# Optimization experiments

Measured on AMD Instinct MI355X. Metric: run time of the kernel, lower is better.

Reference implementation:

```python
import jax, jax.numpy as jnp
import numpy as np

EPS = 1e-5  # BatchNorm3d default eps


def setup_inputs() -> dict:
    key = jax.random.key(0)
    ks = jax.random.split(key, 8)
    B, C, T, H, W = 2, 256, 8, 28, 28
    P, NS = 128, 5
    sc = 0.02  # keep activations stable through 5 residual stages
    return {
        "x": jax.random.normal(ks[0], (B, C, T, H, W), jnp.float32),
        "Wt": jax.random.normal(ks[1], (P, C), jnp.float32) * sc,
        "Wp": jax.random.normal(ks[2], (P, C), jnp.float32) * sc,
        "Wg": jax.random.normal(ks[3], (NS, P, C), jnp.float32) * sc,
        "W1": jax.random.normal(ks[4], (NS, C, P), jnp.float32) * sc,
        "W2": jax.random.normal(ks[5], (NS, C, P), jnp.float32) * sc,
        "gamma": jnp.ones((NS, C), jnp.float32),
        "beta": jnp.zeros((NS, C), jnp.float32),
    }


def _batchnorm(x, g, b):
    # x: [B, C, S]; training-mode BN over (batch, spatial) per channel
    mu = jnp.mean(x, axis=(0, 2), keepdims=True)
    var = jnp.var(x, axis=(0, 2), keepdims=True)
    xn = (x - mu) * jax.lax.rsqrt(var + EPS)
    return xn * g[None, :, None] + b[None, :, None]


def reference(x, Wt, Wp, Wg, W1, W2, gamma, beta):
    B, C, T, H, W = x.shape
    S = T * H * W
    xf = x.reshape(B, C, S)                      # [B,C,S]
    # DotKernel: att[b,i,j] = softmax_j( t[b,i,:] . p[b,:,j] )
    t = jnp.einsum("bcs,pc->bsp", xf, Wt)        # [B,S,P]
    p = jnp.einsum("bcs,pc->bps", xf, Wp)        # [B,P,S]
    att = jax.nn.softmax(jnp.einsum("bsp,bpq->bsq", t, p), axis=-1)  # [B,S,S]

    out = xf
    n_stages = Wg.shape[0]
    for i in range(n_stages):  # small fixed stage count
        g = jnp.einsum("bcs,pc->bsp", out, Wg[i])          # [B,S,P]
        x1 = jnp.einsum("bsp,cp->bcs", g, W1[i])           # w_1(g)
        x2 = jnp.einsum("bsq,bqp->bsp", att, g)            # att @ g
        x2 = jnp.einsum("bsp,cp->bcs", x2, W2[i])          # w_2(...)
        out = _batchnorm(x1 + x2, gamma[i], beta[i]) + out  # BN + residual
    return out.reshape(B, C, T, H, W)
```

## Files before the change

### kernel.cpp

```cpp
#include <hip/hip_runtime.h>

#define B_  2
#define C_  256
#define S_  6272
#define P_  128
#define NS_ 5
#define KS_ 7
#define KCH_ 896
#define EPS_ 1e-5f

typedef __attribute__((ext_vector_type(8))) short short8;
typedef __attribute__((ext_vector_type(4))) float f32x4;

__device__ __forceinline__ ushort f2bf(float f) {
    union { float f; unsigned u; } v; v.f = f;
    unsigned r = v.u + 0x7fffu + ((v.u >> 16) & 1u);
    return (ushort)(r >> 16);
}
__device__ __forceinline__ float bf2f(ushort h) {
    union { unsigned u; float f; } v; v.u = ((unsigned)h) << 16;
    return v.f;
}

__global__ void k_convert_weights(const float* __restrict__ Wt, const float* __restrict__ Wp,
                                  const float* __restrict__ Wg, const float* __restrict__ W1,
                                  const float* __restrict__ W2,
                                  ushort* __restrict__ Wtb, ushort* __restrict__ Wpb,
                                  ushort* __restrict__ Wgb, ushort* __restrict__ catb) {
    int i = blockIdx.x * 256 + threadIdx.x;
    const int nWt  = P_ * C_;
    const int nWg  = NS_ * P_ * C_;
    const int nCat = NS_ * C_ * 2 * P_;
    if (i < nWt) { Wtb[i] = f2bf(Wt[i]); Wpb[i] = f2bf(Wp[i]); }
    if (i < nWg) { Wgb[i] = f2bf(Wg[i]); }
    if (i < nCat) {
        int k  = i & 255;
        int c  = (i >> 8) & (C_ - 1);
        int st = i >> 16;
        float v = (k < P_) ? W1[((size_t)st * C_ + c) * P_ + k]
                           : W2[((size_t)st * C_ + c) * P_ + (k - P_)];
        catb[i] = f2bf(v);
    }
}

__global__ void k_init_x(const float* __restrict__ x, float* __restrict__ out,
                         ushort* __restrict__ xb_sc) {
    int bc = blockIdx.x;
    int b = bc / C_, c = bc - b * C_;
    const float* xr = x + (long)bc * S_;
    float* orow = out + (long)bc * S_;
    ushort* xs = xb_sc + (long)b * S_ * C_;
    for (int s = threadIdx.x; s < S_; s += 256) {
        float v = xr[s];
        orow[s] = v;
        xs[(long)s * C_ + c] = f2bf(v);
    }
}

template <int MODE>
__global__ __launch_bounds__(256, 2)
void k_gemm(const ushort* __restrict__ A, const ushort* __restrict__ Bm,
            void* __restrict__ Out, ushort* __restrict__ OutT,
            int M, int N, int K, int lda, int ldb, int ldo, int ldot,
            long sA, long sB, long sO, long sOT, int nks, int kch) {
    const int z = blockIdx.z;
    const int b = z / nks, ch = z - b * nks;
    A  += (long)b * sA;
    Bm += (long)b * sB;
    const int k0 = ch * kch, k1 = k0 + kch;

    const int bm = blockIdx.x * 128, bn = blockIdx.y * 128;

    __shared__ ushort Al[128][40];
    __shared__ ushort Bl[128][40];

    const int tid = threadIdx.x, lane = tid & 63, wid = tid >> 6;
    const int wr = (wid >> 1) * 64, wc = (wid & 1) * 64;
    const int r16 = lane & 15, kg = lane >> 4;

    f32x4 acc[4][4];
    #pragma unroll
    for (int i = 0; i < 4; ++i)
        #pragma unroll
        for (int j = 0; j < 4; ++j)
            acc[i][j] = (f32x4){0.f, 0.f, 0.f, 0.f};

    for (int kk = k0; kk < k1; kk += 32) {
        {
            int u = tid;         int r = u >> 2, c8 = (u & 3) << 3;
            *(short8*)&Al[r][c8] = *(const short8*)&A[(long)(bm + r) * lda + kk + c8];
        }
        {
            int u = tid + 256;   int r = u >> 2, c8 = (u & 3) << 3;
            *(short8*)&Al[r][c8] = *(const short8*)&A[(long)(bm + r) * lda + kk + c8];
        }
        {
            int u = tid;         int r = u >> 2, c8 = (u & 3) << 3;
            *(short8*)&Bl[r][c8] = *(const short8*)&Bm[(long)(bn + r) * ldb + kk + c8];
        }
        {
            int u = tid + 256;   int r = u >> 2, c8 = (u & 3) << 3;
            *(short8*)&Bl[r][c8] = *(const short8*)&Bm[(long)(bn + r) * ldb + kk + c8];
        }
        __syncthreads();

        short8 af[4], bfv[4];
        #pragma unroll
        for (int i = 0; i < 4; ++i)
            af[i] = *(const short8*)&Al[wr + i * 16 + r16][kg * 8];
        #pragma unroll
        for (int j = 0; j < 4; ++j)
            bfv[j] = *(const short8*)&Bl[wc + j * 16 + r16][kg * 8];

        #pragma unroll
        for (int i = 0; i < 4; ++i)
            #pragma unroll
            for (int j = 0; j < 4; ++j)
                acc[i][j] = __builtin_amdgcn_mfma_f32_16x16x32_bf16(af[i], bfv[j], acc[i][j], 0, 0, 0);
        __syncthreads();
    }

    const int orow0 = bm + wr + kg * 4;
    const int ocol0 = bn + wc + r16;
    if (MODE == 2) {
        float* O = (float*)Out + (long)z * sO;
        #pragma unroll
        for (int i = 0; i < 4; ++i)
            #pragma unroll
            for (int j = 0; j < 4; ++j)
                #pragma unroll
                for (int q = 0; q < 4; ++q)
                    O[(long)(orow0 + i * 16 + q) * ldo + (ocol0 + j * 16)] = acc[i][j][q];
    } else {
        ushort* O = (ushort*)Out + (long)z * sO;
        ushort* OT = (MODE == 1) ? (OutT + (long)z * sOT) : nullptr;
        #pragma unroll
        for (int i = 0; i < 4; ++i)
            #pragma unroll
            for (int j = 0; j < 4; ++j)
                #pragma unroll
                for (int q = 0; q < 4; ++q) {
                    ushort h = f2bf(acc[i][j][q]);
                    O[(long)(orow0 + i * 16 + q) * ldo + (ocol0 + j * 16)] = h;
                    if (MODE == 1)
                        OT[(long)(ocol0 + j * 16) * ldot + (orow0 + i * 16 + q)] = h;
                }
    }
}

__global__ __launch_bounds__(256)
void k_softmax(ushort* __restrict__ att) {
    long row = blockIdx.x;
    ushort* r = att + row * (long)S_;
    const int tid = threadIdx.x;
    __shared__ float red1[4];
    __shared__ float red2[4];

    float v[25];
    float mx = -1e30f;
    #pragma unroll
    for (int i = 0; i < 25; ++i) {
        int idx = i * 256 + tid;
        float xv = (idx < S_) ? bf2f(r[idx]) : -1e30f;
        v[i] = xv;
        mx = fmaxf(mx, xv);
    }
    #pragma unroll
    for (int off = 32; off; off >>= 1) mx = fmaxf(mx, __shfl_xor(mx, off));
    if ((tid & 63) == 0) red1[tid >> 6] = mx;
    __syncthreads();
    mx = fmaxf(fmaxf(red1[0], red1[1]), fmaxf(red1[2], red1[3]));

    float sum = 0.f;
    #pragma unroll
    for (int i = 0; i < 25; ++i) {
        int idx = i * 256 + tid;
        float e = (idx < S_) ? __expf(v[i] - mx) : 0.f;
        v[i] = e;
        sum += e;
    }
    #pragma unroll
    for (int off = 32; off; off >>= 1) sum += __shfl_xor(sum, off);
    if ((tid & 63) == 0) red2[tid >> 6] = sum;
    __syncthreads();
    sum = red2[0] + red2[1] + red2[2] + red2[3];
    float inv = 1.f / sum;

    #pragma unroll
    for (int i = 0; i < 25; ++i) {
        int idx = i * 256 + tid;
        if (idx < S_) r[idx] = f2bf(v[i] * inv);
    }
}

__global__ void k_reduce_split(const float* __restrict__ split, ushort* __restrict__ BcatT) {
    long i = (long)blockIdx.x * 256 + threadIdx.x;
    if (i >= (long)B_ * S_ * P_) return;
    int p = (int)(i & (P_ - 1));
    long sp = i >> 7;
    int b = (int)(sp / S_);
    long s = sp - (long)b * S_;
    const float* base = split + (long)b * KS_ * S_ * P_ + s * P_ + p;
    float acc = 0.f;
    #pragma unroll
    for (int ch = 0; ch < KS_; ++ch) acc += base[(long)ch * S_ * P_];
    BcatT[((long)b * S_ + s) * 256 + 128 + p] = f2bf(acc);
}

__global__ __launch_bounds__(256)
void k_bn_stats(const float* __restrict__ y, float* __restrict__ mu, float* __restrict__ rs) {
    int c = blockIdx.x;
    const int tid = threadIdx.x;
    float s1 = 0.f, s2 = 0.f;
    for (int b = 0; b < B_; ++b) {
        const float* r = y + ((long)b * C_ + c) * S_;
        for (int s = tid; s < S_; s += 256) {
            float v = r[s];
            s1 += v;
            s2 += v * v;
        }
    }
    #pragma unroll
    for (int off = 32; off; off >>= 1) {
        s1 += __shfl_xor(s1, off);
        s2 += __shfl_xor(s2, off);
    }
    __shared__ float a1[4], a2[4];
    if ((tid & 63) == 0) { a1[tid >> 6] = s1; a2[tid >> 6] = s2; }
    __syncthreads();
    if (tid == 0) {
        s1 = a1[0] + a1[1] + a1[2] + a1[3];
        s2 = a2[0] + a2[1] + a2[2] + a2[3];
        const float invn = 1.f / (float)(B_ * S_);
        float m = s1 * invn;
        float var = s2 * invn - m * m;
        mu[c] = m;
        rs[c] = rsqrtf(var + EPS_);
    }
}

__global__ __launch_bounds__(256)
void k_bn_apply(const float* __restrict__ y, const float* __restrict__ mu,
                const float* __restrict__ rs, const float* __restrict__ gamma,
                const float* __restrict__ beta, float* __restrict__ out,
                ushort* __restrict__ xb_sc) {
    int bc = blockIdx.x;
    int b = bc / C_, c = bc - b * C_;
    float m = mu[c], r = rs[c], g = gamma[c], be = beta[c];
    const float* yr = y + (long)bc * S_;
    float* orow = out + (long)bc * S_;
    ushort* xs = xb_sc + (long)b * S_ * C_;
    for (int s = threadIdx.x; s < S_; s += 256) {
        float v = orow[s] + (yr[s] - m) * r * g + be;
        orow[s] = v;
        xs[(long)s * C_ + c] = f2bf(v);
    }
}

extern "C" void kernel_launch(void* const* d_in, const int* in_sizes, int n_in,
                              void* d_out, int out_size, void* d_ws, size_t ws_size,
                              hipStream_t stream) {
    const float* x     = (const float*)d_in[0];
    const float* Wt    = (const float*)d_in[1];
    const float* Wp    = (const float*)d_in[2];
    const float* Wg    = (const float*)d_in[3];
    const float* W1    = (const float*)d_in[4];
    const float* W2    = (const float*)d_in[5];
    const float* gamma = (const float*)d_in[6];
    const float* beta  = (const float*)d_in[7];
    float* out = (float*)d_out;

    char* ws = (char*)d_ws;
    size_t off = 0;
    auto alloc = [&](size_t bytes) -> void* {
        void* p = ws + off;
        off = (off + bytes + 255) & ~(size_t)255;
        return p;
    };
    ushort* att   = (ushort*)alloc((size_t)B_ * S_ * S_ * 2);
    ushort* tb    = (ushort*)alloc((size_t)B_ * S_ * P_ * 2);
    ushort* ptb   = (ushort*)alloc((size_t)B_ * S_ * P_ * 2);
    ushort* gTb   = (ushort*)alloc((size_t)B_ * P_ * S_ * 2);
    ushort* BcatT = (ushort*)alloc((size_t)B_ * S_ * 256 * 2);
    ushort* xbsc  = (ushort*)alloc((size_t)B_ * S_ * C_ * 2);
    float*  y     = (float*)alloc((size_t)B_ * C_ * S_ * 4);
    float*  split = (float*)alloc((size_t)B_ * KS_ * S_ * P_ * 4);
    ushort* Wtb   = (ushort*)alloc((size_t)P_ * C_ * 2);
    ushort* Wpb   = (ushort*)alloc((size_t)P_ * C_ * 2);
    ushort* Wgb   = (ushort*)alloc((size_t)NS_ * P_ * C_ * 2);
    ushort* catb  = (ushort*)alloc((size_t)NS_ * C_ * 256 * 2);
    float*  mu    = (float*)alloc(C_ * 4);
    float*  rs    = (float*)alloc(C_ * 4);
    if (off > ws_size) return;

    dim3 blk(256);

    k_convert_weights<<<1280, 256, 0, stream>>>(Wt, Wp, Wg, W1, W2, Wtb, Wpb, Wgb, catb);
    k_init_x<<<B_ * C_, 256, 0, stream>>>(x, out, xbsc);

    k_gemm<0><<<dim3(S_ / 128, P_ / 128, B_), blk, 0, stream>>>(
        xbsc, Wtb, tb, nullptr, S_, P_, C_, C_, C_, P_, 0,
        (long)S_ * C_, 0, (long)S_ * P_, 0, 1, C_);
    k_gemm<0><<<dim3(S_ / 128, P_ / 128, B_), blk, 0, stream>>>(
        xbsc, Wpb, ptb, nullptr, S_, P_, C_, C_, C_, P_, 0,
        (long)S_ * C_, 0, (long)S_ * P_, 0, 1, C_);
    k_gemm<0><<<dim3(S_ / 128, S_ / 128, B_), blk, 0, stream>>>(
        tb, ptb, att, nullptr, S_, S_, P_, P_, P_, S_, 0,
        (long)S_ * P_, (long)S_ * P_, (long)S_ * S_, 0, 1, P_);
    k_softmax<<<B_ * S_, 256, 0, stream>>>(att);

    for (int i = 0; i < NS_; ++i) {
        k_gemm<1><<<dim3(S_ / 128, P_ / 128, B_), blk, 0, stream>>>(
            xbsc, Wgb + (size_t)i * P_ * C_, BcatT, gTb,
            S_, P_, C_, C_, C_, 256, S_,
            (long)S_ * C_, 0, (long)S_ * 256, (long)P_ * S_, 1, C_);
        k_gemm<2><<<dim3(S_ / 128, P_ / 128, B_ * KS_), blk, 0, stream>>>(
            att, gTb, split, nullptr, S_, P_, S_, S_, S_, P_, 0,
            (long)S_ * S_, (long)P_ * S_, (long)S_ * P_, 0, KS_, KCH_);
        k_reduce_split<<<(int)(((long)B_ * S_ * P_ + 255) / 256), 256, 0, stream>>>(split, BcatT);
        k_gemm<2><<<dim3(C_ / 128, S_ / 128, B_), blk, 0, stream>>>(
            catb + (size_t)i * C_ * 256, BcatT, y, nullptr,
            C_, S_, 256, 256, 256, S_, 0,
            0, (long)S_ * 256, (long)C_ * S_, 0, 1, 256);
        k_bn_stats<<<C_, 256, 0, stream>>>(y, mu, rs);
        k_bn_apply<<<B_ * C_, 256, 0, stream>>>(y, mu, rs, gamma + i * C_, beta + i * C_, out, xbsc);
    }
}
```

Baseline: 760.7 us.

## Use direct global-to-LDS loads with XOR swizzle, fuse t/p projections, vectorize softmax

The GEMM tile loads now use global_load_lds to write straight into unpadded LDS. An XOR swizzle on the k-slot replaces padding to avoid bank conflicts, and the register round trip for staging is removed. The Wt and Wp projections are merged into one GEMM over concatenated weights that writes an interleaved t|p buffer, and the attention GEMM reads both halves through stride 256. Softmax now uses 16-byte vector loads and stores, with 8 contiguous elements per thread instead of strided scalar accesses.

Result: faster. 729.4 us (-4.1%).

```diff
diff --git a/kernel.cpp b/kernel.cpp
--- a/kernel.cpp
+++ b/kernel.cpp
@@ -22,16 +22,26 @@
     return v.f;
 }
 
+__device__ __forceinline__ void gload16(const ushort* g, ushort* lds) {
+    __builtin_amdgcn_global_load_lds(
+        (const __attribute__((address_space(1))) void*)g,
+        (__attribute__((address_space(3))) void*)lds, 16, 0, 0);
+}
+
 __global__ void k_convert_weights(const float* __restrict__ Wt, const float* __restrict__ Wp,
                                   const float* __restrict__ Wg, const float* __restrict__ W1,
                                   const float* __restrict__ W2,
-                                  ushort* __restrict__ Wtb, ushort* __restrict__ Wpb,
+                                  ushort* __restrict__ Wtpb,
                                   ushort* __restrict__ Wgb, ushort* __restrict__ catb) {
     int i = blockIdx.x * 256 + threadIdx.x;
-    const int nWt  = P_ * C_;
+    const int nWtp = 2 * P_ * C_;
     const int nWg  = NS_ * P_ * C_;
     const int nCat = NS_ * C_ * 2 * P_;
-    if (i < nWt) { Wtb[i] = f2bf(Wt[i]); Wpb[i] = f2bf(Wp[i]); }
+    if (i < nWtp) {
+        int c = i & (C_ - 1), row = i >> 8;
+        float v = (row < P_) ? Wt[row * C_ + c] : Wp[(row - P_) * C_ + c];
+        Wtpb[i] = f2bf(v);
+    }
     if (i < nWg) { Wgb[i] = f2bf(Wg[i]); }
     if (i < nCat) {
         int k  = i & 255;
@@ -71,13 +81,23 @@
 
     const int bm = blockIdx.x * 128, bn = blockIdx.y * 128;
 
-    __shared__ ushort Al[128][40];
-    __shared__ ushort Bl[128][40];
+    __shared__ ushort Al[128][32];
+    __shared__ ushort Bl[128][32];
 
     const int tid = threadIdx.x, lane = tid & 63, wid = tid >> 6;
     const int wr = (wid >> 1) * 64, wc = (wid & 1) * 64;
     const int r16 = lane & 15, kg = lane >> 4;
 
+    const int st_row = lane >> 2;
+    const int st_slot = lane & 3;
+    const int st_gk8 = ((st_slot ^ ((st_row >> 1) & 3)) << 3);
+    const int sw8 = ((kg ^ ((r16 >> 1) & 3)) << 3);
+
+    const ushort* Arow0 = A + (long)(bm + wid * 32 + st_row) * lda + st_gk8;
+    const ushort* Arow1 = A + (long)(bm + wid * 32 + 16 + st_row) * lda + st_gk8;
+    const ushort* Brow0 = Bm + (long)(bn + wid * 32 + st_row) * ldb + st_gk8;
+    const ushort* Brow1 = Bm + (long)(bn + wid * 32 + 16 + st_row) * ldb + st_gk8;
+
     f32x4 acc[4][4];
     #pragma unroll
     for (int i = 0; i < 4; ++i)
@@ -86,31 +106,19 @@
             acc[i][j] = (f32x4){0.f, 0.f, 0.f, 0.f};
 
     for (int kk = k0; kk < k1; kk += 32) {
-        {
-            int u = tid;         int r = u >> 2, c8 = (u & 3) << 3;
-            *(short8*)&Al[r][c8] = *(const short8*)&A[(long)(bm + r) * lda + kk + c8];
-        }
-        {
-            int u = tid + 256;   int r = u >> 2, c8 = (u & 3) << 3;
-            *(short8*)&Al[r][c8] = *(const short8*)&A[(long)(bm + r) * lda + kk + c8];
-        }
-        {
-            int u = tid;         int r = u >> 2, c8 = (u & 3) << 3;
-            *(short8*)&Bl[r][c8] = *(const short8*)&Bm[(long)(bn + r) * ldb + kk + c8];
-        }
-        {
-            int u = tid + 256;   int r = u >> 2, c8 = (u & 3) << 3;
-            *(short8*)&Bl[r][c8] = *(const short8*)&Bm[(long)(bn + r) * ldb + kk + c8];
-        }
+        gload16(Arow0 + kk, &Al[wid * 32][0]);
+        gload16(Arow1 + kk, &Al[wid * 32 + 16][0]);
+        gload16(Brow0 + kk, &Bl[wid * 32][0]);
+        gload16(Brow1 + kk, &Bl[wid * 32 + 16][0]);
         __syncthreads();
 
         short8 af[4], bfv[4];
         #pragma unroll
         for (int i = 0; i < 4; ++i)
-            af[i] = *(const short8*)&Al[wr + i * 16 + r16][kg * 8];
+            af[i] = *(const short8*)&Al[wr + i * 16 + r16][sw8];
         #pragma unroll
         for (int j = 0; j < 4; ++j)
-            bfv[j] = *(const short8*)&Bl[wc + j * 16 + r16][kg * 8];
+            bfv[j] = *(const short8*)&Bl[wc + j * 16 + r16][sw8];
 
         #pragma unroll
         for (int i = 0; i < 4; ++i)
@@ -155,16 +163,24 @@
     const int tid = threadIdx.x;
     __shared__ float red1[4];
     __shared__ float red2[4];
-
-    float v[25];
+    const bool tail = tid < 16;
+
+    short8 u0 = *(const short8*)&r[(0 * 256 + tid) * 8];
+    short8 u1 = *(const short8*)&r[(1 * 256 + tid) * 8];
+    short8 u2 = *(const short8*)&r[(2 * 256 + tid) * 8];
+    short8 u3 = tail ? *(const short8*)&r[(768 + tid) * 8] : short8{0,0,0,0,0,0,0,0};
+
+    float v[32];
+    #pragma unroll
+    for (int j = 0; j < 8; ++j) {
+        v[j]      = bf2f((ushort)u0[j]);
+        v[8 + j]  = bf2f((ushort)u1[j]);
+        v[16 + j] = bf2f((ushort)u2[j]);
+        v[24 + j] = tail ? bf2f((ushort)u3[j]) : -1e30f;
+    }
     float mx = -1e30f;
     #pragma unroll
-    for (int i = 0; i < 25; ++i) {
-        int idx = i * 256 + tid;
-        float xv = (idx < S_) ? bf2f(r[idx]) : -1e30f;
-        v[i] = xv;
-        mx = fmaxf(mx, xv);
-    }
+    for (int j = 0; j < 32; ++j) mx = fmaxf(mx, v[j]);
     #pragma unroll
     for (int off = 32; off; off >>= 1) mx = fmaxf(mx, __shfl_xor(mx, off));
     if ((tid & 63) == 0) red1[tid >> 6] = mx;
@@ -173,10 +189,9 @@
 
     float sum = 0.f;
     #pragma unroll
-    for (int i = 0; i < 25; ++i) {
-        int idx = i * 256 + tid;
-        float e = (idx < S_) ? __expf(v[i] - mx) : 0.f;
-        v[i] = e;
+    for (int j = 0; j < 32; ++j) {
+        float e = __expf(v[j] - mx);
+        v[j] = e;
         sum += e;
     }
     #pragma unroll
@@ -186,11 +201,18 @@
     sum = red2[0] + red2[1] + red2[2] + red2[3];
     float inv = 1.f / sum;
 
-    #pragma unroll
-    for (int i = 0; i < 25; ++i) {
-        int idx = i * 256 + tid;
-        if (idx < S_) r[idx] = f2bf(v[i] * inv);
-    }
+    short8 w0, w1, w2, w3;
+    #pragma unroll
+    for (int j = 0; j < 8; ++j) {
+        w0[j] = (short)f2bf(v[j] * inv);
+        w1[j] = (short)f2bf(v[8 + j] * inv);
+        w2[j] = (short)f2bf(v[16 + j] * inv);
+        w3[j] = (short)f2bf(v[24 + j] * inv);
+    }
+    *(short8*)&r[(0 * 256 + tid) * 8] = w0;
+    *(short8*)&r[(1 * 256 + tid) * 8] = w1;
+    *(short8*)&r[(2 * 256 + tid) * 8] = w2;
+    if (tail) *(short8*)&r[(768 + tid) * 8] = w3;
 }
 
 __global__ void k_reduce_split(const float* __restrict__ split, ushort* __restrict__ BcatT) {
@@ -278,15 +300,13 @@
         return p;
     };
     ushort* att   = (ushort*)alloc((size_t)B_ * S_ * S_ * 2);
-    ushort* tb    = (ushort*)alloc((size_t)B_ * S_ * P_ * 2);
-    ushort* ptb   = (ushort*)alloc((size_t)B_ * S_ * P_ * 2);
+    ushort* tpb   = (ushort*)alloc((size_t)B_ * S_ * 256 * 2);
     ushort* gTb   = (ushort*)alloc((size_t)B_ * P_ * S_ * 2);
     ushort* BcatT = (ushort*)alloc((size_t)B_ * S_ * 256 * 2);
     ushort* xbsc  = (ushort*)alloc((size_t)B_ * S_ * C_ * 2);
     float*  y     = (float*)alloc((size_t)B_ * C_ * S_ * 4);
     float*  split = (float*)alloc((size_t)B_ * KS_ * S_ * P_ * 4);
-    ushort* Wtb   = (ushort*)alloc((size_t)P_ * C_ * 2);
-    ushort* Wpb   = (ushort*)alloc((size_t)P_ * C_ * 2);
+    ushort* Wtpb  = (ushort*)alloc((size_t)2 * P_ * C_ * 2);
     ushort* Wgb   = (ushort*)alloc((size_t)NS_ * P_ * C_ * 2);
     ushort* catb  = (ushort*)alloc((size_t)NS_ * C_ * 256 * 2);
     float*  mu    = (float*)alloc(C_ * 4);
@@ -295,26 +315,23 @@
 
     dim3 blk(256);
 
-    k_convert_weights<<<1280, 256, 0, stream>>>(Wt, Wp, Wg, W1, W2, Wtb, Wpb, Wgb, catb);
+    k_convert_weights<<<1280, 256, 0, stream>>>(Wt, Wp, Wg, W1, W2, Wtpb, Wgb, catb);
     k_init_x<<<B_ * C_, 256, 0, stream>>>(x, out, xbsc);
 
-    k_gemm<0><<<dim3(S_ / 128, P_ / 128, B_), blk, 0, stream>>>(
-        xbsc, Wtb, tb, nullptr, S_, P_, C_, C_, C_, P_, 0,
-        (long)S_ * C_, 0, (long)S_ * P_, 0, 1, C_);
-    k_gemm<0><<<dim3(S_ / 128, P_ / 128, B_), blk, 0, stream>>>(
-        xbsc, Wpb, ptb, nullptr, S_, P_, C_, C_, C_, P_, 0,
-        (long)S_ * C_, 0, (long)S_ * P_, 0, 1, C_);
+    k_gemm<0><<<dim3(S_ / 128, 2, B_), blk, 0, stream>>>(
+        xbsc, Wtpb, tpb, nullptr, S_, 256, C_, C_, C_, 256, 0,
+        (long)S_ * C_, 0, (long)S_ * 256, 0, 1, C_);
     k_gemm<0><<<dim3(S_ / 128, S_ / 128, B_), blk, 0, stream>>>(
-        tb, ptb, att, nullptr, S_, S_, P_, P_, P_, S_, 0,
-        (long)S_ * P_, (long)S_ * P_, (long)S_ * S_, 0, 1, P_);
+        tpb, tpb + 128, att, nullptr, S_, S_, P_, 256, 256, S_, 0,
+        (long)S_ * 256, (long)S_ * 256, (long)S_ * S_, 0, 1, P_);
     k_softmax<<<B_ * S_, 256, 0, stream>>>(att);
 
     for (int i = 0; i < NS_; ++i) {
-        k_gemm<1><<<dim3(S_ / 128, P_ / 128, B_), blk, 0, stream>>>(
+        k_gemm<1><<<dim3(S_ / 128, 1, B_), blk, 0, stream>>>(
             xbsc, Wgb + (size_t)i * P_ * C_, BcatT, gTb,
             S_, P_, C_, C_, C_, 256, S_,
             (long)S_ * C_, 0, (long)S_ * 256, (long)P_ * S_, 1, C_);
-        k_gemm<2><<<dim3(S_ / 128, P_ / 128, B_ * KS_), blk, 0, stream>>>(
+        k_gemm<2><<<dim3(S_ / 128, 1, B_ * KS_), blk, 0, stream>>>(
             att, gTb, split, nullptr, S_, P_, S_, S_, S_, P_, 0,
             (long)S_ * S_, (long)P_ * S_, (long)S_ * P_, 0, KS_, KCH_);
         k_reduce_split<<<(int)(((long)B_ * S_ * P_ + 255) / 256), 256, 0, stream>>>(split, BcatT);
```
